# Kernel tuning notes

Measured on AMD Instinct MI355X. Metric: run time of the kernel, lower is better.

The kernel has to match this reference:

```python
import jax, jax.numpy as jnp
import numpy as np

DIM = 320
NUM_HEADS = 5
HEAD_DIM = DIM // NUM_HEADS  # 64
SCALE = HEAD_DIM ** -0.5


def setup_inputs() -> dict:
    key = jax.random.key(0)
    k1, k2, k3, k4 = jax.random.split(key, 4)
    B, N, C = 8, 2048, DIM
    x = jax.random.normal(k1, (B, N, C), dtype=jnp.float32)
    # nn.Linear(dim, dim*3, bias=False): weight [3*dim, dim]
    w_qkv = jax.random.normal(k2, (3 * C, C), dtype=jnp.float32) * (C ** -0.5)
    # nn.Linear(dim, dim): weight [dim, dim], bias [dim]
    w_proj = jax.random.normal(k3, (C, C), dtype=jnp.float32) * (C ** -0.5)
    b_proj = jax.random.normal(k4, (C,), dtype=jnp.float32) * 0.01
    return {"x": x, "w_qkv": w_qkv, "w_proj": w_proj, "b_proj": b_proj}


def reference(x, w_qkv, w_proj, b_proj):
    B, N, C = x.shape
    H, D = NUM_HEADS, HEAD_DIM
    # qkv projection: [B, N, 3C] -> [3, B, H, N, D]
    qkv = jnp.einsum('bnc,kc->bnk', x, w_qkv)
    qkv = qkv.reshape(B, N, 3, H, D).transpose(2, 0, 3, 1, 4)
    q, k, v = qkv[0], qkv[1], qkv[2]
    # full attention matrix [B, H, N, N] (retained by original module)
    attn = jnp.einsum('bhnd,bhmd->bhnm', q, k) * SCALE
    attn = jax.nn.softmax(attn, axis=-1)
    # attn_drop p=0 -> identity (eval/deterministic)
    out = jnp.einsum('bhnm,bhmd->bhnd', attn, v)
    out = out.transpose(0, 2, 1, 3).reshape(B, N, C)
    out = jnp.einsum('bnc,oc->bno', out, w_proj) + b_proj
    # proj_drop p=0 -> identity
    return out
```

## Files before the change

### kernel.cpp

```cpp
#include <hip/hip_runtime.h>
#include <hip/hip_bf16.h>


typedef __attribute__((ext_vector_type(8))) short bf16x8;
typedef __attribute__((ext_vector_type(4))) float f32x4;

#define MFMA(a, b, c) __builtin_amdgcn_mfma_f32_16x16x32_bf16((a), (b), (c), 0, 0, 0)

#define QSCALE 0.18033688322643216f

static __device__ __forceinline__ bf16x8 ld8(const __hip_bfloat16* p) {
    return *reinterpret_cast<const bf16x8*>(p);
}

static __device__ __forceinline__ void split_bf16(float v, __hip_bfloat16& h,
                                                  __hip_bfloat16& l) {
    __hip_bfloat16 hh = __float2bfloat16(v);
    h = hh;
    l = __float2bfloat16(v - __bfloat162float(hh));
}

__global__ __launch_bounds__(256)
void split_inputs(const float* __restrict__ x, const float* __restrict__ wq,
                  const float* __restrict__ wp,
                  __hip_bfloat16* __restrict__ xb, __hip_bfloat16* __restrict__ wqb,
                  __hip_bfloat16* __restrict__ wph, __hip_bfloat16* __restrict__ wpl)
{
    const size_t tid = (size_t)blockIdx.x * blockDim.x + threadIdx.x;
    const size_t stride = (size_t)gridDim.x * blockDim.x;
    const float4* x4 = (const float4*)x;
    ushort4* xb4 = (ushort4*)xb;
    for (size_t i = tid; i < 1310720u; i += stride) {
        float4 v = x4[i];
        __hip_bfloat16 b0 = __float2bfloat16(v.x), b1 = __float2bfloat16(v.y);
        __hip_bfloat16 b2 = __float2bfloat16(v.z), b3 = __float2bfloat16(v.w);
        ushort4 u;
        u.x = *reinterpret_cast<unsigned short*>(&b0);
        u.y = *reinterpret_cast<unsigned short*>(&b1);
        u.z = *reinterpret_cast<unsigned short*>(&b2);
        u.w = *reinterpret_cast<unsigned short*>(&b3);
        xb4[i] = u;
    }
    for (size_t i = tid; i < 307200u; i += stride) wqb[i] = __float2bfloat16(wq[i]);
    for (size_t i = tid; i < 102400u; i += stride) split_bf16(wp[i], wph[i], wpl[i]);
}

__global__ __launch_bounds__(256)
void qkv_kernel(const __hip_bfloat16* __restrict__ x,
                const __hip_bfloat16* __restrict__ w,
                __hip_bfloat16* __restrict__ qout,
                __hip_bfloat16* __restrict__ kp,
                __hip_bfloat16* __restrict__ vp)
{
    __shared__ __align__(16) __hip_bfloat16 As[128 * 72];
    __shared__ __align__(16) __hip_bfloat16 Bs[64 * 72];

    const int tid  = threadIdx.x;
    const int wv   = tid >> 6;
    const int lane = tid & 63;
    const int quad = lane >> 4;
    const int col  = lane & 15;
    const int m0   = blockIdx.x * 128;
    const int n0   = blockIdx.y * 64;

    f32x4 acc[2][4];
#pragma unroll
    for (int i = 0; i < 2; ++i)
#pragma unroll
        for (int j = 0; j < 4; ++j) acc[i][j] = (f32x4){0.f, 0.f, 0.f, 0.f};

    for (int k0 = 0; k0 < 320; k0 += 64) {
        __syncthreads();
#pragma unroll
        for (int i = 0; i < 4; ++i) {
            int ch = tid + i * 256;
            int r = ch >> 3, sg = ch & 7;
            *reinterpret_cast<float4*>(&As[r * 72 + sg * 8]) =
                *reinterpret_cast<const float4*>(&x[(m0 + r) * 320 + k0 + sg * 8]);
        }
#pragma unroll
        for (int i = 0; i < 2; ++i) {
            int ch = tid + i * 256;
            int r = ch >> 3, sg = ch & 7;
            *reinterpret_cast<float4*>(&Bs[r * 72 + sg * 8]) =
                *reinterpret_cast<const float4*>(&w[(n0 + r) * 320 + k0 + sg * 8]);
        }
        __syncthreads();

#pragma unroll
        for (int hf = 0; hf < 2; ++hf) {
            bf16x8 a0 = ld8(&As[(wv * 32 + col) * 72 + hf * 32 + quad * 8]);
            bf16x8 a1 = ld8(&As[(wv * 32 + 16 + col) * 72 + hf * 32 + quad * 8]);
#pragma unroll
            for (int nt = 0; nt < 4; ++nt) {
                bf16x8 b = ld8(&Bs[(nt * 16 + col) * 72 + hf * 32 + quad * 8]);
                acc[0][nt] = MFMA(a0, b, acc[0][nt]);
                acc[1][nt] = MFMA(a1, b, acc[1][nt]);
            }
        }
    }

    const int s = blockIdx.y / 5;
    const int h = blockIdx.y % 5;
#pragma unroll
    for (int mt = 0; mt < 2; ++mt) {
#pragma unroll
        for (int nt = 0; nt < 4; ++nt) {
#pragma unroll
            for (int r = 0; r < 4; ++r) {
                int m = m0 + wv * 32 + mt * 16 + quad * 4 + r;
                int d = nt * 16 + col;
                int b = m >> 11, n = m & 2047;
                int bh = b * 5 + h;
                float val = acc[mt][nt][r];
                if (s == 0) {
                    qout[((size_t)bh * 2048 + n) * 64 + d] =
                        __float2bfloat16(val * QSCALE);
                } else if (s == 1) {
                    int p = n >> 6, nn = n & 63;
                    size_t a = ((size_t)(bh * 32 + p) * 8 + (d >> 5) * 4 + (nn >> 4)) * 512
                             + (((d >> 3) & 3) * 16 + (nn & 15)) * 8 + (d & 7);
                    kp[a] = __float2bfloat16(val);
                } else {
                    int p = n >> 6;
                    size_t a = ((size_t)(bh * 32 + p) * 8 + ((n >> 5) & 1) * 4 + (d >> 4)) * 512
                             + (((n >> 3) & 3) * 16 + (d & 15)) * 8 + (n & 7);
                    vp[a] = __float2bfloat16(val);
                }
            }
        }
    }
}

__global__ __launch_bounds__(64)
void attn_kernel(const __hip_bfloat16* __restrict__ Q,
                 const __hip_bfloat16* __restrict__ Kp,
                 const __hip_bfloat16* __restrict__ Vp,
                 __hip_bfloat16* __restrict__ A2h,
                 __hip_bfloat16* __restrict__ A2l)
{
    __shared__ __align__(16) __hip_bfloat16 Ps[32 * 72];

    const int lane = threadIdx.x;
    const int quad = lane >> 4;
    const int col  = lane & 15;
    const int bh = blockIdx.y, b = bh / 5, h = bh % 5;
    const __hip_bfloat16* Qh = Q + (size_t)bh * 2048 * 64;
    const __hip_bfloat16* Kh = Kp + (size_t)bh * 32 * 8 * 512;
    const __hip_bfloat16* Vh = Vp + (size_t)bh * 32 * 8 * 512;
    const int q0 = blockIdx.x * 32;

    bf16x8 qf[2][2];
#pragma unroll
    for (int mt = 0; mt < 2; ++mt)
#pragma unroll
        for (int hf = 0; hf < 2; ++hf)
            qf[mt][hf] = ld8(&Qh[(q0 + mt * 16 + col) * 64 + hf * 32 + quad * 8]);

    f32x4 lp[2];
    f32x4 o[2][4];
#pragma unroll
    for (int mt = 0; mt < 2; ++mt) {
        lp[mt] = (f32x4){0.f, 0.f, 0.f, 0.f};
#pragma unroll
        for (int dt = 0; dt < 4; ++dt) o[mt][dt] = (f32x4){0.f, 0.f, 0.f, 0.f};
    }

    bf16x8 ka[8], va[8];
#pragma unroll
    for (int f = 0; f < 8; ++f) ka[f] = ld8(&Kh[(size_t)f * 512 + lane * 8]);
#pragma unroll
    for (int f = 0; f < 8; ++f) va[f] = ld8(&Vh[(size_t)f * 512 + lane * 8]);

    for (int t = 0; t < 32; ++t) {
        const int tn = (t < 31) ? (t + 1) : 31;

        f32x4 s[2][4];
#pragma unroll
        for (int mt = 0; mt < 2; ++mt)
#pragma unroll
            for (int nt = 0; nt < 4; ++nt) {
                f32x4 z = (f32x4){0.f, 0.f, 0.f, 0.f};
                z = MFMA(qf[mt][0], ka[nt], z);
                z = MFMA(qf[mt][1], ka[4 + nt], z);
                s[mt][nt] = z;
            }

#pragma unroll
        for (int f = 0; f < 8; ++f)
            ka[f] = ld8(&Kh[((size_t)tn * 8 + f) * 512 + lane * 8]);

#pragma unroll
        for (int mt = 0; mt < 2; ++mt)
#pragma unroll
            for (int nt = 0; nt < 4; ++nt) {
                f32x4 pv;
#pragma unroll
                for (int r = 0; r < 4; ++r)
                    pv[r] = __builtin_amdgcn_exp2f(s[mt][nt][r]);
                lp[mt] += pv;
#pragma unroll
                for (int r = 0; r < 4; ++r)
                    Ps[(mt * 16 + quad * 4 + r) * 72 + ((nt ^ quad) * 16) + col] =
                        __float2bfloat16(pv[r]);
            }
        __asm__ volatile("s_waitcnt lgkmcnt(0)" ::: "memory");

#pragma unroll
        for (int mt = 0; mt < 2; ++mt)
#pragma unroll
            for (int kk = 0; kk < 2; ++kk) {
                int g = (kk * 2 + (quad >> 1)) ^ ((col >> 2) & 3);
                bf16x8 pf = ld8(&Ps[(mt * 16 + col) * 72 + g * 16 + (quad & 1) * 8]);
#pragma unroll
                for (int dt = 0; dt < 4; ++dt)
                    o[mt][dt] = MFMA(pf, va[kk * 4 + dt], o[mt][dt]);
            }

#pragma unroll
        for (int f = 0; f < 8; ++f)
            va[f] = ld8(&Vh[((size_t)tn * 8 + f) * 512 + lane * 8]);
    }

    float l_fin[2][4];
#pragma unroll
    for (int mt = 0; mt < 2; ++mt)
#pragma unroll
        for (int r = 0; r < 4; ++r) {
            float v = lp[mt][r];
#pragma unroll
            for (int off = 1; off < 16; off <<= 1)
                v += __shfl_xor(v, off, 64);
            l_fin[mt][r] = v;
        }

#pragma unroll
    for (int mt = 0; mt < 2; ++mt) {
#pragma unroll
        for (int r = 0; r < 4; ++r) {
            float inv = 1.0f / l_fin[mt][r];
            int row = q0 + mt * 16 + quad * 4 + r;
#pragma unroll
            for (int dt = 0; dt < 4; ++dt) {
                int d = dt * 16 + col;
                size_t idx = ((size_t)(b * 2048 + row)) * 320 + h * 64 + d;
                split_bf16(o[mt][dt][r] * inv, A2h[idx], A2l[idx]);
            }
        }
    }
}

__global__ __launch_bounds__(256)
void proj_kernel(const __hip_bfloat16* __restrict__ ah, const __hip_bfloat16* __restrict__ al,
                 const __hip_bfloat16* __restrict__ wh, const __hip_bfloat16* __restrict__ wl,
                 const float* __restrict__ bias,
                 float* __restrict__ out)
{
    __shared__ __align__(16) __hip_bfloat16 Ash[128 * 40];
    __shared__ __align__(16) __hip_bfloat16 Asl[128 * 40];
    __shared__ __align__(16) __hip_bfloat16 Bsh[64 * 40];
    __shared__ __align__(16) __hip_bfloat16 Bsl[64 * 40];

    const int tid  = threadIdx.x;
    const int wv   = tid >> 6;
    const int lane = tid & 63;
    const int quad = lane >> 4;
    const int col  = lane & 15;
    const int m0   = blockIdx.x * 128;
    const int n0   = blockIdx.y * 64;

    f32x4 acc[2][4];
#pragma unroll
    for (int i = 0; i < 2; ++i)
#pragma unroll
        for (int j = 0; j < 4; ++j) acc[i][j] = (f32x4){0.f, 0.f, 0.f, 0.f};

    for (int k0 = 0; k0 < 320; k0 += 32) {
        __syncthreads();
#pragma unroll
        for (int i = 0; i < 2; ++i) {
            int ch = tid + i * 256;
            int r = ch >> 2, sg = ch & 3;
            *reinterpret_cast<float4*>(&Ash[r * 40 + sg * 8]) =
                *reinterpret_cast<const float4*>(&ah[(m0 + r) * 320 + k0 + sg * 8]);
            *reinterpret_cast<float4*>(&Asl[r * 40 + sg * 8]) =
                *reinterpret_cast<const float4*>(&al[(m0 + r) * 320 + k0 + sg * 8]);
        }
        {
            int r = tid >> 2, sg = tid & 3;
            *reinterpret_cast<float4*>(&Bsh[r * 40 + sg * 8]) =
                *reinterpret_cast<const float4*>(&wh[(n0 + r) * 320 + k0 + sg * 8]);
            *reinterpret_cast<float4*>(&Bsl[r * 40 + sg * 8]) =
                *reinterpret_cast<const float4*>(&wl[(n0 + r) * 320 + k0 + sg * 8]);
        }
        __syncthreads();

        bf16x8 a0h = ld8(&Ash[(wv * 32 + col) * 40 + quad * 8]);
        bf16x8 a1h = ld8(&Ash[(wv * 32 + 16 + col) * 40 + quad * 8]);
        bf16x8 a0l = ld8(&Asl[(wv * 32 + col) * 40 + quad * 8]);
        bf16x8 a1l = ld8(&Asl[(wv * 32 + 16 + col) * 40 + quad * 8]);
#pragma unroll
        for (int nt = 0; nt < 4; ++nt) {
            bf16x8 bh = ld8(&Bsh[(nt * 16 + col) * 40 + quad * 8]);
            bf16x8 bl = ld8(&Bsl[(nt * 16 + col) * 40 + quad * 8]);
            acc[0][nt] = MFMA(a0h, bh, acc[0][nt]);
            acc[0][nt] = MFMA(a0h, bl, acc[0][nt]);
            acc[0][nt] = MFMA(a0l, bh, acc[0][nt]);
            acc[1][nt] = MFMA(a1h, bh, acc[1][nt]);
            acc[1][nt] = MFMA(a1h, bl, acc[1][nt]);
            acc[1][nt] = MFMA(a1l, bh, acc[1][nt]);
        }
    }

#pragma unroll
    for (int nt = 0; nt < 4; ++nt) {
        float bv = bias[n0 + nt * 16 + col];
#pragma unroll
        for (int mt = 0; mt < 2; ++mt) {
#pragma unroll
            for (int r = 0; r < 4; ++r) {
                int m = m0 + wv * 32 + mt * 16 + quad * 4 + r;
                out[(size_t)m * 320 + n0 + nt * 16 + col] = acc[mt][nt][r] + bv;
            }
        }
    }
}

extern "C" void kernel_launch(void* const* d_in, const int* in_sizes, int n_in,
                              void* d_out, int out_size, void* d_ws, size_t ws_size,
                              hipStream_t stream)
{
    const float* x      = (const float*)d_in[0];
    const float* w_qkv  = (const float*)d_in[1];
    const float* w_proj = (const float*)d_in[2];
    const float* b_proj = (const float*)d_in[3];
    float* out = (float*)d_out;

    const size_t NX = 5242880, NWQ = 307200, NWP = 102400;
    __hip_bfloat16* xb  = (__hip_bfloat16*)d_ws;
    __hip_bfloat16* wqb = xb + NX;
    __hip_bfloat16* wph = wqb + NWQ;
    __hip_bfloat16* wpl = wph + NWP;
    __hip_bfloat16* q   = wpl + NWP;
    __hip_bfloat16* kp  = q + NX;
    __hip_bfloat16* vp  = kp + NX;
    __hip_bfloat16* a2l = vp + NX;
    __hip_bfloat16* a2h = xb;

    split_inputs<<<1024, 256, 0, stream>>>(x, w_qkv, w_proj, xb, wqb, wph, wpl);
    qkv_kernel<<<dim3(128, 15), 256, 0, stream>>>(xb, wqb, q, kp, vp);
    attn_kernel<<<dim3(64, 40), 64, 0, stream>>>(q, kp, vp, a2h, a2l);
    proj_kernel<<<dim3(128, 5), 256, 0, stream>>>(a2h, a2l, wph, wpl, b_proj, out);
}
```

Baseline: 207.4 us.

## Split attention key range across two waves and merge partial results in LDS

Each attention block now runs two wavefronts. Each wave processes half of the key tiles with its own P scratch area, and the two partial outputs and row sums are combined through shared memory before normalisation and store. The goal is twice the in-flight waves for the same grid, to hide memory and MFMA latency. The V loads move from a one-tile-ahead prefetch to a load in the same iteration, which may expose load latency. Q fragments are loaded twice per block, and there is a sync plus a reduction epilogue. Because the kernel skips the max subtraction in softmax, summing the two partials directly stays correct.

```diff
diff --git a/kernel.cpp b/kernel.cpp
--- a/kernel.cpp
+++ b/kernel.cpp
@@ -132,16 +132,18 @@
     }
 }
 
-__global__ __launch_bounds__(64)
+__global__ __launch_bounds__(128, 4)
 void attn_kernel(const __hip_bfloat16* __restrict__ Q,
                  const __hip_bfloat16* __restrict__ Kp,
                  const __hip_bfloat16* __restrict__ Vp,
                  __hip_bfloat16* __restrict__ A2h,
                  __hip_bfloat16* __restrict__ A2l)
 {
-    __shared__ __align__(16) __hip_bfloat16 Ps[32 * 72];
-
-    const int lane = threadIdx.x;
+    __shared__ __align__(16) unsigned char smraw[9216];
+
+    const int tid  = threadIdx.x;
+    const int wv   = tid >> 6;
+    const int lane = tid & 63;
     const int quad = lane >> 4;
     const int col  = lane & 15;
     const int bh = blockIdx.y, b = bh / 5, h = bh % 5;
@@ -150,6 +152,8 @@
     const __hip_bfloat16* Vh = Vp + (size_t)bh * 32 * 8 * 512;
     const int q0 = blockIdx.x * 32;
 
+    __hip_bfloat16* Ps = (__hip_bfloat16*)smraw + wv * 2304;
+
     bf16x8 qf[2][2];
 #pragma unroll
     for (int mt = 0; mt < 2; ++mt)
@@ -166,14 +170,15 @@
         for (int dt = 0; dt < 4; ++dt) o[mt][dt] = (f32x4){0.f, 0.f, 0.f, 0.f};
     }
 
-    bf16x8 ka[8], va[8];
-#pragma unroll
-    for (int f = 0; f < 8; ++f) ka[f] = ld8(&Kh[(size_t)f * 512 + lane * 8]);
-#pragma unroll
-    for (int f = 0; f < 8; ++f) va[f] = ld8(&Vh[(size_t)f * 512 + lane * 8]);
-
-    for (int t = 0; t < 32; ++t) {
-        const int tn = (t < 31) ? (t + 1) : 31;
+    const int t0 = wv * 16, t1 = t0 + 16;
+
+    bf16x8 ka[8];
+#pragma unroll
+    for (int f = 0; f < 8; ++f)
+        ka[f] = ld8(&Kh[((size_t)t0 * 8 + f) * 512 + lane * 8]);
+
+    for (int t = t0; t < t1; ++t) {
+        const int tn = (t + 1 < t1) ? (t + 1) : t;
 
         f32x4 s[2][4];
 #pragma unroll
@@ -186,6 +191,11 @@
                 s[mt][nt] = z;
             }
 
+        bf16x8 va[8];
+#pragma unroll
+        for (int f = 0; f < 8; ++f)
+            va[f] = ld8(&Vh[((size_t)t * 8 + f) * 512 + lane * 8]);
+
 #pragma unroll
         for (int f = 0; f < 8; ++f)
             ka[f] = ld8(&Kh[((size_t)tn * 8 + f) * 512 + lane * 8]);
@@ -216,13 +226,9 @@
                 for (int dt = 0; dt < 4; ++dt)
                     o[mt][dt] = MFMA(pf, va[kk * 4 + dt], o[mt][dt]);
             }
-
-#pragma unroll
-        for (int f = 0; f < 8; ++f)
-            va[f] = ld8(&Vh[((size_t)tn * 8 + f) * 512 + lane * 8]);
-    }
-
-    float l_fin[2][4];
+    }
+
+    float lval[2][4];
 #pragma unroll
     for (int mt = 0; mt < 2; ++mt)
 #pragma unroll
@@ -231,20 +237,43 @@
 #pragma unroll
             for (int off = 1; off < 16; off <<= 1)
                 v += __shfl_xor(v, off, 64);
-            l_fin[mt][r] = v;
-        }
-
-#pragma unroll
-    for (int mt = 0; mt < 2; ++mt) {
-#pragma unroll
-        for (int r = 0; r < 4; ++r) {
-            float inv = 1.0f / l_fin[mt][r];
-            int row = q0 + mt * 16 + quad * 4 + r;
-#pragma unroll
-            for (int dt = 0; dt < 4; ++dt) {
-                int d = dt * 16 + col;
-                size_t idx = ((size_t)(b * 2048 + row)) * 320 + h * 64 + d;
-                split_bf16(o[mt][dt][r] * inv, A2h[idx], A2l[idx]);
+            lval[mt][r] = v;
+        }
+
+    float* cbo = (float*)smraw;
+    float* cbl = cbo + 2048;
+    __syncthreads();
+    if (wv == 1) {
+#pragma unroll
+        for (int mt = 0; mt < 2; ++mt)
+#pragma unroll
+            for (int dt = 0; dt < 4; ++dt)
+#pragma unroll
+                for (int r = 0; r < 4; ++r)
+                    cbo[(mt * 16 + quad * 4 + r) * 64 + dt * 16 + col] = o[mt][dt][r];
+        if (col == 0)
+#pragma unroll
+            for (int mt = 0; mt < 2; ++mt)
+#pragma unroll
+                for (int r = 0; r < 4; ++r)
+                    cbl[mt * 16 + quad * 4 + r] = lval[mt][r];
+    }
+    __syncthreads();
+    if (wv == 0) {
+#pragma unroll
+        for (int mt = 0; mt < 2; ++mt) {
+#pragma unroll
+            for (int r = 0; r < 4; ++r) {
+                int row = mt * 16 + quad * 4 + r;
+                float inv = 1.0f / (lval[mt][r] + cbl[row]);
+                int grow = q0 + row;
+#pragma unroll
+                for (int dt = 0; dt < 4; ++dt) {
+                    int d = dt * 16 + col;
+                    float val = (o[mt][dt][r] + cbo[row * 64 + d]) * inv;
+                    size_t idx = ((size_t)(b * 2048 + grow)) * 320 + h * 64 + d;
+                    split_bf16(val, A2h[idx], A2l[idx]);
+                }
             }
         }
     }
@@ -349,6 +378,6 @@
 
     split_inputs<<<1024, 256, 0, stream>>>(x, w_qkv, w_proj, xb, wqb, wph, wpl);
     qkv_kernel<<<dim3(128, 15), 256, 0, stream>>>(xb, wqb, q, kp, vp);
-    attn_kernel<<<dim3(64, 40), 64, 0, stream>>>(q, kp, vp, a2h, a2l);
+    attn_kernel<<<dim3(64, 40), 128, 0, stream>>>(q, kp, vp, a2h, a2l);
     proj_kernel<<<dim3(128, 5), 256, 0, stream>>>(a2h, a2l, wph, wpl, b_proj, out);
 }
```

New measurement: 395.7 us. 1.91x slower.
